# Kernel tuning notes

Hardware: AMD Instinct MI355X
Metric: run time of the kernel (lower is better)

Reference implementation:

```python
import jax, jax.numpy as jnp
import numpy as np

D_MODEL = 512
NHEAD = 8
HEAD_DIM = D_MODEL // NHEAD


def setup_inputs() -> dict:
    key = jax.random.key(0)
    k1, k2, k3, k4, k5 = jax.random.split(key, 5)
    x = jax.random.normal(k1, (4, 2048, D_MODEL), dtype=jnp.float32)
    s = 1.0 / np.sqrt(D_MODEL)
    W_qkv = jax.random.normal(k2, (D_MODEL, 3 * D_MODEL), dtype=jnp.float32) * s
    b_qkv = jax.random.normal(k3, (3 * D_MODEL,), dtype=jnp.float32) * 0.01
    W_fc = jax.random.normal(k4, (D_MODEL, D_MODEL), dtype=jnp.float32) * s
    b_fc = jax.random.normal(k5, (D_MODEL,), dtype=jnp.float32) * 0.01
    return {"x": x, "W_qkv": W_qkv, "b_qkv": b_qkv, "W_fc": W_fc, "b_fc": b_fc}


def reference(x, W_qkv, b_qkv, W_fc, b_fc):
    b, t, _ = x.shape
    qkv = x @ W_qkv + b_qkv                      # [b, t, 3*d]
    q, k, v = jnp.split(qkv, 3, axis=-1)
    def heads(a):
        return a.reshape(b, t, NHEAD, HEAD_DIM).transpose(0, 2, 1, 3)  # b h t d
    q, k, v = heads(q), heads(k), heads(v)
    scale = HEAD_DIM ** -0.5
    dots = jnp.einsum('bhid,bhjd->bhij', q, k) * scale
    attn = jax.nn.softmax(dots, axis=-1)         # dropout = identity (eval)
    out = jnp.einsum('bhij,bhjd->bhid', attn, v)
    out = out.transpose(0, 2, 1, 3).reshape(b, t, D_MODEL)
    return out @ W_fc + b_fc
```

## Files before the change

kernel.cpp:

```cpp
#include <hip/hip_runtime.h>
#include <hip/hip_bf16.h>
#include <cstddef>
#include <cstdint>

typedef __bf16 bf16_t;
typedef __attribute__((ext_vector_type(8))) __bf16 bf16x8;
typedef __attribute__((ext_vector_type(4))) float f32x4;
typedef __attribute__((ext_vector_type(16))) float f32x16;
typedef __attribute__((ext_vector_type(2))) unsigned uint2v;

#define B_   4
#define T_   2048
#define D_   512
#define H_   8
#define HD_  64
#define BT_  8192
#define N3_  1536

__device__ inline f32x4 mfma16(bf16x8 a, bf16x8 b, f32x4 c) {
  return __builtin_amdgcn_mfma_f32_16x16x32_bf16(a, b, c, 0, 0, 0);
}
__device__ inline f32x16 mfma32(bf16x8 a, bf16x8 b, f32x16 c) {
  return __builtin_amdgcn_mfma_f32_32x32x16_bf16(a, b, c, 0, 0, 0);
}

#define GLOADLDS(lds_base, gsrc)                                           \
  __builtin_amdgcn_global_load_lds(                                        \
      (const __attribute__((address_space(1))) unsigned int*)(gsrc),       \
      (__attribute__((address_space(3))) unsigned int*)(lds_base), 16, 0, 0)


__global__ __launch_bounds__(256) void k_castx(const float* __restrict__ in,
                                               bf16_t* __restrict__ out) {
  const size_t i = ((size_t)blockIdx.x * 256 + threadIdx.x) * 8;
  f32x4 v0 = *reinterpret_cast<const f32x4*>(&in[i]);
  f32x4 v1 = *reinterpret_cast<const f32x4*>(&in[i + 4]);
  bf16x8 o;
#pragma unroll
  for (int k = 0; k < 4; ++k) { o[k] = (bf16_t)v0[k]; o[4 + k] = (bf16_t)v1[k]; }
  *reinterpret_cast<bf16x8*>(&out[i]) = o;
}

__global__ __launch_bounds__(256) void k_tcast(const float* __restrict__ in,
                                               bf16_t* __restrict__ out,
                                               int R, int C) {
  __shared__ bf16_t tile[64][72];
  const int c0 = blockIdx.x * 64, r0 = blockIdx.y * 64;
  const int t = threadIdx.x;
  const int rr = t >> 4;
  const int cc = (t & 15) * 4;
#pragma unroll
  for (int p = 0; p < 4; ++p) {
    int r = p * 16 + rr;
    f32x4 v = *reinterpret_cast<const f32x4*>(&in[(size_t)(r0 + r) * C + c0 + cc]);
#pragma unroll
    for (int i = 0; i < 4; ++i) tile[cc + i][r] = (bf16_t)v[i];
  }
  __syncthreads();
#pragma unroll
  for (int p = 0; p < 4; ++p) {
    int c = p * 16 + rr;
    union { uint2 u; bf16_t e[4]; } pk;
#pragma unroll
    for (int i = 0; i < 4; ++i) pk.e[i] = tile[c][cc + i];
    *reinterpret_cast<uint2*>(&out[(size_t)(c0 + c) * R + r0 + cc]) = pk.u;
  }
}

__global__ __launch_bounds__(512) void k_gemm_qkv(
    const bf16_t* __restrict__ Xb, const bf16_t* __restrict__ Wt,
    const float* __restrict__ bias, bf16_t* __restrict__ Qp,
    bf16_t* __restrict__ Kp, bf16_t* __restrict__ Vp) {
  __shared__ __align__(16) bf16_t As[128 * 32];
  __shared__ __align__(16) bf16_t Bs[128 * 32];
  const int bm0 = blockIdx.x * 128, bn0 = blockIdx.y * 128;
  const int tid = threadIdx.x, lane = tid & 63, wid = tid >> 6;
  const int wm = wid >> 1, wn = wid & 1;
  const int srow = 16 * wid + (lane >> 2);
  const int scol = (lane & 3) * 8;
  f32x4 acc[2][4] = {};
  for (int kt = 0; kt < D_; kt += 32) {
    GLOADLDS(&As[(16 * wid) * 32], &Xb[(size_t)(bm0 + srow) * D_ + kt + scol]);
    GLOADLDS(&Bs[(16 * wid) * 32], &Wt[(size_t)(bn0 + srow) * D_ + kt + scol]);
    __syncthreads();
    const int fr = lane & 15, kq = (lane >> 4) * 8;
    bf16x8 af[2], bfr[4];
#pragma unroll
    for (int m = 0; m < 2; ++m)
      af[m] = *reinterpret_cast<const bf16x8*>(&As[(wm * 32 + m * 16 + fr) * 32 + kq]);
#pragma unroll
    for (int n = 0; n < 4; ++n)
      bfr[n] = *reinterpret_cast<const bf16x8*>(&Bs[(wn * 64 + n * 16 + fr) * 32 + kq]);
#pragma unroll
    for (int m = 0; m < 2; ++m)
#pragma unroll
      for (int n = 0; n < 4; ++n)
        acc[m][n] = mfma16(af[m], bfr[n], acc[m][n]);
    __syncthreads();
  }
  const float c1 = 0.18033688011112042f;
  const int fr = lane & 15, fq = lane >> 4;
#pragma unroll
  for (int n = 0; n < 4; ++n) {
    int ng = bn0 + wn * 64 + n * 16 + fr;
    float bv = bias[ng];
    int sec = ng >> 9, ns = ng & 511;
    int h = ns >> 6, d = ns & 63;
#pragma unroll
    for (int m = 0; m < 2; ++m) {
      int mg = bm0 + wm * 32 + m * 16 + fq * 4;
      if (sec == 2) {
        int tt = mg & 2047, bb = mg >> 11;
        int bh = bb * H_ + h;
        union { uint2 u; bf16_t e[4]; } pk;
#pragma unroll
        for (int j = 0; j < 4; ++j) pk.e[j] = (bf16_t)(acc[m][n][j] + bv);
        size_t a = (((size_t)(bh * 128 + (tt >> 4)) * 2 + (d >> 5)) << 9) +
                   (size_t)((d & 31) + 32 * ((tt >> 3) & 1)) * 8 + (tt & 7);
        *reinterpret_cast<uint2*>(&Vp[a]) = pk.u;
      } else {
#pragma unroll
        for (int j = 0; j < 4; ++j) {
          int row = mg + j;
          int bb = row >> 11, tt = row & 2047;
          int bh = bb * H_ + h;
          float fv = acc[m][n][j] + bv;
          size_t a = (((size_t)(bh * 64 + (tt >> 5)) * 4 + (d >> 4)) << 9) +
                     (size_t)((tt & 31) + 32 * ((d >> 3) & 1)) * 8 + (d & 7);
          (sec == 0 ? Qp : Kp)[a] = (bf16_t)(sec == 0 ? fv * c1 : fv);
        }
      }
    }
  }
}

__global__ __launch_bounds__(512) void k_gemm_fc(
    const bf16_t* __restrict__ A, const bf16_t* __restrict__ Wt,
    const float* __restrict__ bias, float* __restrict__ Out) {
  __shared__ __align__(16) bf16_t As[128 * 32];
  __shared__ __align__(16) bf16_t Bs[128 * 32];
  const int bm0 = blockIdx.x * 128, bn0 = blockIdx.y * 128;
  const int tid = threadIdx.x, lane = tid & 63, wid = tid >> 6;
  const int wm = wid >> 1, wn = wid & 1;
  const int srow = 16 * wid + (lane >> 2);
  const int scol = (lane & 3) * 8;
  f32x4 acc[2][4] = {};
  for (int kt = 0; kt < D_; kt += 32) {
    GLOADLDS(&As[(16 * wid) * 32], &A[(size_t)(bm0 + srow) * D_ + kt + scol]);
    GLOADLDS(&Bs[(16 * wid) * 32], &Wt[(size_t)(bn0 + srow) * D_ + kt + scol]);
    __syncthreads();
    const int fr = lane & 15, kq = (lane >> 4) * 8;
    bf16x8 af[2], bfr[4];
#pragma unroll
    for (int m = 0; m < 2; ++m)
      af[m] = *reinterpret_cast<const bf16x8*>(&As[(wm * 32 + m * 16 + fr) * 32 + kq]);
#pragma unroll
    for (int n = 0; n < 4; ++n)
      bfr[n] = *reinterpret_cast<const bf16x8*>(&Bs[(wn * 64 + n * 16 + fr) * 32 + kq]);
#pragma unroll
    for (int m = 0; m < 2; ++m)
#pragma unroll
      for (int n = 0; n < 4; ++n)
        acc[m][n] = mfma16(af[m], bfr[n], acc[m][n]);
    __syncthreads();
  }
  const int fr = lane & 15, fq = lane >> 4;
#pragma unroll
  for (int n = 0; n < 4; ++n) {
    int ng = bn0 + wn * 64 + n * 16 + fr;
    float bv = bias[ng];
#pragma unroll
    for (int m = 0; m < 2; ++m) {
      int mg = bm0 + wm * 32 + m * 16 + fq * 4;
#pragma unroll
      for (int j = 0; j < 4; ++j)
        Out[(size_t)(mg + j) * D_ + ng] = acc[m][n][j] + bv;
    }
  }
}

__device__ __forceinline__ void loadKf(const bf16_t* __restrict__ b, int tile,
                                       bf16x8 (&kf)[4]) {
#pragma unroll
  for (int ds = 0; ds < 4; ++ds)
    kf[ds] = *reinterpret_cast<const bf16x8*>(b + ((size_t)(tile * 4 + ds) << 9));
}
__device__ __forceinline__ void loadVf(const bf16_t* __restrict__ b, int c0,
                                       bf16x8 (&v)[4]) {
  v[0] = *reinterpret_cast<const bf16x8*>(b + ((size_t)(c0 * 2 + 0) << 9));
  v[1] = *reinterpret_cast<const bf16x8*>(b + ((size_t)(c0 * 2 + 2) << 9));
  v[2] = *reinterpret_cast<const bf16x8*>(b + ((size_t)(c0 * 2 + 1) << 9));
  v[3] = *reinterpret_cast<const bf16x8*>(b + ((size_t)(c0 * 2 + 3) << 9));
}

__device__ __forceinline__ f32x16 qk32(const bf16x8 (&kf)[4],
                                       const bf16x8 (&qf)[4]) {
  f32x16 s;
#pragma unroll
  for (int i = 0; i < 16; ++i) s[i] = 0.f;
  __builtin_amdgcn_s_setprio(1);
  s = mfma32(kf[0], qf[0], s);
  s = mfma32(kf[1], qf[1], s);
  s = mfma32(kf[2], qf[2], s);
  s = mfma32(kf[3], qf[3], s);
  __builtin_amdgcn_s_setprio(0);
  return s;
}

__device__ __forceinline__ void pv_acc(f32x16& s, const bf16x8 (&v)[4],
                                       f32x16& o0, f32x16& o1, float& lsum) {
  float p[16];
#pragma unroll
  for (int r = 0; r < 16; ++r) p[r] = __builtin_exp2f(s[r]);
  lsum += (((p[0] + p[1]) + (p[2] + p[3])) + ((p[4] + p[5]) + (p[6] + p[7]))) +
          (((p[8] + p[9]) + (p[10] + p[11])) +
           ((p[12] + p[13]) + (p[14] + p[15])));
  union PW { __hip_bfloat162 h; unsigned u; };
#pragma unroll
  for (int ks = 0; ks < 2; ++ks) {
    const int rb = ks * 8;
    PW t0, t1, t2, t3;
    t0.h = __float22bfloat162_rn(make_float2(p[rb + 0], p[rb + 1]));
    t1.h = __float22bfloat162_rn(make_float2(p[rb + 2], p[rb + 3]));
    t2.h = __float22bfloat162_rn(make_float2(p[rb + 4], p[rb + 5]));
    t3.h = __float22bfloat162_rn(make_float2(p[rb + 6], p[rb + 7]));
    uint2v r02 = __builtin_amdgcn_permlane32_swap(t0.u, t2.u, false, false);
    uint2v r13 = __builtin_amdgcn_permlane32_swap(t1.u, t3.u, false, false);
    union { unsigned u[4]; bf16x8 vv; } af;
    af.u[0] = r02[0]; af.u[1] = r13[0]; af.u[2] = r02[1]; af.u[3] = r13[1];
    __builtin_amdgcn_s_setprio(1);
    if (ks == 0) {
      o0 = mfma32(af.vv, v[0], o0);
      o1 = mfma32(af.vv, v[2], o1);
    } else {
      o0 = mfma32(af.vv, v[1], o0);
      o1 = mfma32(af.vv, v[3], o1);
    }
    __builtin_amdgcn_s_setprio(0);
  }
}

__global__ __launch_bounds__(256, 2) void k_attn(
    const bf16_t* __restrict__ Qp, const bf16_t* __restrict__ Kp,
    const bf16_t* __restrict__ Vp, bf16_t* __restrict__ Ctx) {
  __shared__ float Olds[3][32][64];
  __shared__ float Llds[3][64];
  const int lin = blockIdx.x;
  const int logical = (lin & 7) * 256 + (lin >> 3);
  const int bh = logical >> 6, qblk = logical & 63;
  const int tid = threadIdx.x, lane = tid & 63, half = tid >> 6;
  const int tbase = half * 16;
  const bf16_t* Qb = Qp + ((size_t)(bh * 64 + qblk) << 11) + lane * 8;
  const bf16_t* Kb = Kp + ((size_t)bh << 17) + lane * 8;
  const bf16_t* Vb = Vp + ((size_t)bh << 17) + lane * 8;
  bf16x8 qf[4];
#pragma unroll
  for (int ds = 0; ds < 4; ++ds)
    qf[ds] = *reinterpret_cast<const bf16x8*>(Qb + ((size_t)ds << 9));
  f32x16 o0, o1;
#pragma unroll
  for (int i = 0; i < 16; ++i) { o0[i] = 0.f; o1[i] = 0.f; }
  float lsum = 0.f;
  bf16x8 kfA[4], kfB[4], vA[4], vB[4];
  loadKf(Kb, tbase + 0, kfA);
  loadKf(Kb, tbase + 1, kfB);
  loadVf(Vb, (tbase + 0) * 2, vA);
  loadVf(Vb, (tbase + 1) * 2, vB);
  f32x16 sA = qk32(kfA, qf);
  for (int st = 0; st < 16; st += 2) {
    const bool more = (st + 2 < 16);
    f32x16 sB = qk32(kfB, qf);
    if (more) loadKf(Kb, tbase + st + 2, kfA);
    pv_acc(sA, vA, o0, o1, lsum);
    if (more) loadVf(Vb, (tbase + st + 2) * 2, vA);
    if (more) sA = qk32(kfA, qf);
    if (more) loadKf(Kb, tbase + st + 3, kfB);
    pv_acc(sB, vB, o0, o1, lsum);
    if (more) loadVf(Vb, (tbase + st + 3) * 2, vB);
  }
  lsum += __shfl_xor(lsum, 32);
  if (half > 0) {
#pragma unroll
    for (int r = 0; r < 16; ++r) {
      Olds[half - 1][r][lane] = o0[r];
      Olds[half - 1][16 + r][lane] = o1[r];
    }
    Llds[half - 1][lane] = lsum;
  }
  __syncthreads();
  if (half > 0) return;
  const float lfull =
      lsum + Llds[0][lane] + Llds[1][lane] + Llds[2][lane];
  const float linv = 1.f / lfull;
  const int bb = bh >> 3, hh = bh & 7;
  const int ql = lane & 31;
  const int q0 = qblk * 32;
#pragma unroll
  for (int r = 0; r < 16; ++r) {
    const int qr = (r & 3) + 8 * (r >> 2) + 4 * (lane >> 5);
    const float li = __shfl(linv, qr);
    float v0 = (o0[r] + Olds[0][r][lane] + Olds[1][r][lane] +
                Olds[2][r][lane]) * li;
    float v1 = (o1[r] + Olds[0][16 + r][lane] + Olds[1][16 + r][lane] +
                Olds[2][16 + r][lane]) * li;
    size_t base = ((size_t)(bb * T_ + q0 + qr)) * D_ + hh * HD_ + ql;
    Ctx[base] = (bf16_t)v0;
    Ctx[base + 32] = (bf16_t)v1;
  }
}

extern "C" void kernel_launch(void* const* d_in, const int* in_sizes, int n_in,
                              void* d_out, int out_size, void* d_ws,
                              size_t ws_size, hipStream_t stream) {
  const float* x    = (const float*)d_in[0];
  const float* Wqkv = (const float*)d_in[1];
  const float* bqkv = (const float*)d_in[2];
  const float* Wfc  = (const float*)d_in[3];
  const float* bfc  = (const float*)d_in[4];
  float* out = (float*)d_out;

  char* ws = (char*)d_ws;
  size_t off = 0;
  bf16_t* Wqt = (bf16_t*)(ws + off); off += (size_t)N3_ * D_ * 2;
  bf16_t* Wft = (bf16_t*)(ws + off); off += (size_t)D_ * D_ * 2;
  bf16_t* Qb  = (bf16_t*)(ws + off); off += (size_t)BT_ * D_ * 2;
  bf16_t* Kb  = (bf16_t*)(ws + off); off += (size_t)BT_ * D_ * 2;
  bf16_t* Vb  = (bf16_t*)(ws + off); off += (size_t)BT_ * D_ * 2;
  bf16_t* Ctx = (bf16_t*)(ws + off); off += (size_t)BT_ * D_ * 2;
  bf16_t* Xb  = Ctx;

  k_castx<<<BT_ * D_ / (256 * 8), 256, 0, stream>>>(x, Xb);
  k_tcast<<<dim3(N3_ / 64, D_ / 64), 256, 0, stream>>>(Wqkv, Wqt, D_, N3_);
  k_tcast<<<dim3(D_ / 64, D_ / 64), 256, 0, stream>>>(Wfc, Wft, D_, D_);
  k_gemm_qkv<<<dim3(BT_ / 128, N3_ / 128), 512, 0, stream>>>(Xb, Wqt, bqkv, Qb,
                                                             Kb, Vb);
  k_attn<<<2048, 256, 0, stream>>>(Qb, Kb, Vb, Ctx);
  k_gemm_fc<<<dim3(BT_ / 128, D_ / 128), 512, 0, stream>>>(Ctx, Wft, bfc, out);
}
```

Baseline: 114.6 us.

## Share K/V tiles across query waves via double-buffered LDS in attention

The attention kernel now has each of the four waves handle a different 32-query block and stream the whole key sequence. K/V tiles are staged once per block into double-buffered LDS with global-to-LDS loads, replacing the old scheme where waves split the key range and each wave read K/V from global memory into registers. This removes the cross-wave LDS reduction of partial outputs and sums, and cuts global K/V traffic by sharing tiles among the four waves. In exchange it adds a block-wide barrier per tile, reduces the grid from 2048 to 512 blocks, and gives each wave a longer serial key loop.

```diff
diff --git a/kernel.cpp b/kernel.cpp
--- a/kernel.cpp
+++ b/kernel.cpp
@@ -177,20 +177,6 @@
         Out[(size_t)(mg + j) * D_ + ng] = acc[m][n][j] + bv;
     }
   }
-}
-
-__device__ __forceinline__ void loadKf(const bf16_t* __restrict__ b, int tile,
-                                       bf16x8 (&kf)[4]) {
-#pragma unroll
-  for (int ds = 0; ds < 4; ++ds)
-    kf[ds] = *reinterpret_cast<const bf16x8*>(b + ((size_t)(tile * 4 + ds) << 9));
-}
-__device__ __forceinline__ void loadVf(const bf16_t* __restrict__ b, int c0,
-                                       bf16x8 (&v)[4]) {
-  v[0] = *reinterpret_cast<const bf16x8*>(b + ((size_t)(c0 * 2 + 0) << 9));
-  v[1] = *reinterpret_cast<const bf16x8*>(b + ((size_t)(c0 * 2 + 2) << 9));
-  v[2] = *reinterpret_cast<const bf16x8*>(b + ((size_t)(c0 * 2 + 1) << 9));
-  v[3] = *reinterpret_cast<const bf16x8*>(b + ((size_t)(c0 * 2 + 3) << 9));
 }
 
 __device__ __forceinline__ f32x16 qk32(const bf16x8 (&kf)[4],
@@ -243,16 +229,19 @@
 __global__ __launch_bounds__(256, 2) void k_attn(
     const bf16_t* __restrict__ Qp, const bf16_t* __restrict__ Kp,
     const bf16_t* __restrict__ Vp, bf16_t* __restrict__ Ctx) {
-  __shared__ float Olds[3][32][64];
-  __shared__ float Llds[3][64];
+  __shared__ __align__(16) bf16_t Ks[2][4096];
+  __shared__ __align__(16) bf16_t Vs[2][4096];
   const int lin = blockIdx.x;
-  const int logical = (lin & 7) * 256 + (lin >> 3);
-  const int bh = logical >> 6, qblk = logical & 63;
-  const int tid = threadIdx.x, lane = tid & 63, half = tid >> 6;
-  const int tbase = half * 16;
-  const bf16_t* Qb = Qp + ((size_t)(bh * 64 + qblk) << 11) + lane * 8;
-  const bf16_t* Kb = Kp + ((size_t)bh << 17) + lane * 8;
-  const bf16_t* Vb = Vp + ((size_t)bh << 17) + lane * 8;
+  const int logical = (lin & 7) * 64 + (lin >> 3);
+  const int bh = logical >> 4, qblk = logical & 15;
+  const int tid = threadIdx.x, lane = tid & 63, wid = tid >> 6;
+  const int q0 = qblk * 128 + wid * 32;
+  const bf16_t* Qb =
+      Qp + ((size_t)(bh * 64 + qblk * 4 + wid) << 11) + lane * 8;
+  const bf16_t* KbE = Kp + ((size_t)bh << 17);
+  const bf16_t* VbE = Vp + ((size_t)bh << 17);
+  const int ldst = wid * 1024;
+  const int soff = ldst + lane * 8;
   bf16x8 qf[4];
 #pragma unroll
   for (int ds = 0; ds < 4; ++ds)
@@ -261,51 +250,48 @@
 #pragma unroll
   for (int i = 0; i < 16; ++i) { o0[i] = 0.f; o1[i] = 0.f; }
   float lsum = 0.f;
-  bf16x8 kfA[4], kfB[4], vA[4], vB[4];
-  loadKf(Kb, tbase + 0, kfA);
-  loadKf(Kb, tbase + 1, kfB);
-  loadVf(Vb, (tbase + 0) * 2, vA);
-  loadVf(Vb, (tbase + 1) * 2, vB);
-  f32x16 sA = qk32(kfA, qf);
-  for (int st = 0; st < 16; st += 2) {
-    const bool more = (st + 2 < 16);
-    f32x16 sB = qk32(kfB, qf);
-    if (more) loadKf(Kb, tbase + st + 2, kfA);
-    pv_acc(sA, vA, o0, o1, lsum);
-    if (more) loadVf(Vb, (tbase + st + 2) * 2, vA);
-    if (more) sA = qk32(kfA, qf);
-    if (more) loadKf(Kb, tbase + st + 3, kfB);
-    pv_acc(sB, vB, o0, o1, lsum);
-    if (more) loadVf(Vb, (tbase + st + 3) * 2, vB);
+  GLOADLDS(&Ks[0][ldst], KbE + soff);
+  GLOADLDS(&Ks[0][ldst + 512], KbE + soff + 512);
+  GLOADLDS(&Vs[0][ldst], VbE + soff);
+  GLOADLDS(&Vs[0][ldst + 512], VbE + soff + 512);
+  __syncthreads();
+  int buf = 0;
+  for (int t = 0; t < 32; ++t) {
+    if (t + 1 < 32) {
+      const size_t g = (size_t)(t + 1) * 4096 + soff;
+      GLOADLDS(&Ks[buf ^ 1][ldst], KbE + g);
+      GLOADLDS(&Ks[buf ^ 1][ldst + 512], KbE + g + 512);
+      GLOADLDS(&Vs[buf ^ 1][ldst], VbE + g);
+      GLOADLDS(&Vs[buf ^ 1][ldst + 512], VbE + g + 512);
+    }
+#pragma unroll
+    for (int s = 0; s < 2; ++s) {
+      bf16x8 kf[4], vf[4];
+#pragma unroll
+      for (int ds = 0; ds < 4; ++ds)
+        kf[ds] = *reinterpret_cast<const bf16x8*>(
+            &Ks[buf][s * 2048 + ds * 512 + lane * 8]);
+      vf[0] = *reinterpret_cast<const bf16x8*>(&Vs[buf][(4 * s + 0) * 512 + lane * 8]);
+      vf[1] = *reinterpret_cast<const bf16x8*>(&Vs[buf][(4 * s + 2) * 512 + lane * 8]);
+      vf[2] = *reinterpret_cast<const bf16x8*>(&Vs[buf][(4 * s + 1) * 512 + lane * 8]);
+      vf[3] = *reinterpret_cast<const bf16x8*>(&Vs[buf][(4 * s + 3) * 512 + lane * 8]);
+      f32x16 sc = qk32(kf, qf);
+      pv_acc(sc, vf, o0, o1, lsum);
+    }
+    __syncthreads();
+    buf ^= 1;
   }
   lsum += __shfl_xor(lsum, 32);
-  if (half > 0) {
-#pragma unroll
-    for (int r = 0; r < 16; ++r) {
-      Olds[half - 1][r][lane] = o0[r];
-      Olds[half - 1][16 + r][lane] = o1[r];
-    }
-    Llds[half - 1][lane] = lsum;
-  }
-  __syncthreads();
-  if (half > 0) return;
-  const float lfull =
-      lsum + Llds[0][lane] + Llds[1][lane] + Llds[2][lane];
-  const float linv = 1.f / lfull;
+  const float linv = 1.f / lsum;
   const int bb = bh >> 3, hh = bh & 7;
   const int ql = lane & 31;
-  const int q0 = qblk * 32;
 #pragma unroll
   for (int r = 0; r < 16; ++r) {
     const int qr = (r & 3) + 8 * (r >> 2) + 4 * (lane >> 5);
     const float li = __shfl(linv, qr);
-    float v0 = (o0[r] + Olds[0][r][lane] + Olds[1][r][lane] +
-                Olds[2][r][lane]) * li;
-    float v1 = (o1[r] + Olds[0][16 + r][lane] + Olds[1][16 + r][lane] +
-                Olds[2][16 + r][lane]) * li;
     size_t base = ((size_t)(bb * T_ + q0 + qr)) * D_ + hh * HD_ + ql;
-    Ctx[base] = (bf16_t)v0;
-    Ctx[base + 32] = (bf16_t)v1;
+    Ctx[base] = (bf16_t)(o0[r] * li);
+    Ctx[base + 32] = (bf16_t)(o1[r] * li);
   }
 }
 
@@ -334,6 +320,6 @@
   k_tcast<<<dim3(D_ / 64, D_ / 64), 256, 0, stream>>>(Wfc, Wft, D_, D_);
   k_gemm_qkv<<<dim3(BT_ / 128, N3_ / 128), 512, 0, stream>>>(Xb, Wqt, bqkv, Qb,
                                                              Kb, Vb);
-  k_attn<<<2048, 256, 0, stream>>>(Qb, Kb, Vb, Ctx);
+  k_attn<<<512, 256, 0, stream>>>(Qb, Kb, Vb, Ctx);
   k_gemm_fc<<<dim3(BT_ / 128, D_ / 128), 512, 0, stream>>>(Ctx, Wft, bfc, out);
 }
```

After: 121.5 us. +6.0%, slower.
